# Optimization experiments

Measured on AMD Instinct MI355X. Metric: run time of the kernel, lower is better.

The kernel has to match this reference:

```python
import jax, jax.numpy as jnp
import numpy as np

B, T, D, C = 2, 2048, 1024, 10
F = D // 2 + 1  # rfft bins; permutations act on frequency bins (perm_freq=True)


def setup_inputs() -> dict:
    key = jax.random.key(0)
    ks = jax.random.split(key, 6)
    s = 1.0 / np.sqrt(D)
    x = jax.random.normal(ks[0], (B, T, D), jnp.float32)
    Wq = jax.random.normal(ks[1], (D, D), jnp.float32) * s
    Wk = jax.random.normal(ks[2], (D, D), jnp.float32) * s
    Wv = jax.random.normal(ks[3], (D, D), jnp.float32) * s
    Wo = jax.random.normal(ks[4], (D, D), jnp.float32) * s
    # buffer: torch.randn(C, F).argsort(-1) -> random permutations of freq bins
    perms = jnp.argsort(jax.random.normal(ks[5], (C, F)), axis=-1)
    return {"x": x, "Wq": Wq, "Wk": Wk, "Wv": Wv, "Wo": Wo, "perms": perms}


def reference(x, Wq, Wk, Wv, Wo, perms):
    # linear projections (nn.Linear applies x @ W.T)
    q = x @ Wq.T
    k = x @ Wk.T
    v = x @ Wv.T
    # HRR bind/unbind in rfft frequency domain
    fq = jnp.fft.rfft(q, axis=-1)  # (B,T,F) complex
    fk = jnp.fft.rfft(k, axis=-1)
    fv = jnp.fft.rfft(v, axis=-1)
    # gather permuted redundant copies of freq bins: (B,T,C,F) -> (C,B,T,F)
    fkp = jnp.moveaxis(fk[..., perms], 2, 0)
    fqp = jnp.moveaxis(fq[..., perms], 2, 0)
    # causal associative memory: cumulative sum of key*value bindings over time
    kv = jnp.cumsum(fkp * fv[None], axis=-2)  # (C,B,T,F)
    # unbind with query (circular correlation = multiply by conj), mean copies
    r = jnp.mean(kv * jnp.conj(fqp), axis=0)  # (B,T,F)
    values_hat = jnp.fft.irfft(r, n=D, axis=-1)  # (B,T,D)
    return values_hat @ Wo.T
```

## Files before the change

kernel.cpp:

```cpp
#include <hip/hip_runtime.h>
#include <math.h>

#define B_   2
#define T_   2048
#define D_   1024
#define C_   10
#define F_   513
#define NTOK (B_ * T_)
#define LF   3078
#define LFP  3136
#define KP2  1056
#define NCH  128
#define TC   (T_ / NCH)

typedef unsigned short us16;
typedef __attribute__((ext_vector_type(8))) __bf16 bf16x8;
typedef __attribute__((ext_vector_type(4))) float  f32x4;

#define O_XBF    ((size_t)0)
#define O_PREP   ((size_t)8388608)
#define O_WT     (O_PREP)
#define O_WOBF   (O_PREP + 6291456)
#define O_TCS    (O_PREP + 8388608)
#define O_RCAT   (O_PREP)
#define O_SFB    (O_PREP + 10489856)
#define O_MALLB  (O_SFB + 2162688)
#define O_MOUTB  (O_MALLB + 6303744)
#define O_FALL   (O_MOUTB + 2162688)
#define O_SSCAN  (O_FALL + 25690112)

__device__ __forceinline__ us16 f2b(float f) {
    union { float f; unsigned u; } v; v.f = f;
    unsigned r = v.u + 0x7FFFu + ((v.u >> 16) & 1u);
    return (us16)(r >> 16);
}

__device__ __forceinline__ float2 b2f2(unsigned w) {
    union { unsigned u; float f; } a, b;
    a.u = (w & 0xffffu) << 16;
    b.u = w & 0xffff0000u;
    return make_float2(a.f, b.f);
}

__device__ __forceinline__ void gl_lds16(const us16* g, us16* l) {
    __builtin_amdgcn_global_load_lds(
        (const __attribute__((address_space(1))) unsigned*)g,
        (__attribute__((address_space(3))) unsigned*)l, 16, 0, 0);
}

__global__ __launch_bounds__(256)
void hrr_prep(const float* __restrict__ x,  const float* __restrict__ Wq,
              const float* __restrict__ Wk, const float* __restrict__ Wv,
              const float* __restrict__ Wo,
              us16* __restrict__ Xbf, us16* __restrict__ WT,
              us16* __restrict__ WoBf, us16* __restrict__ Tcs,
              us16* __restrict__ Sfb) {
    __shared__ float t[32][33];
    const int bid = blockIdx.x, tid = threadIdx.x;
    if (bid < 4096) {
        int i = bid * 256 + tid;
        float4 v = ((const float4*)x)[i];
        ushort4 o;
        o.x = f2b(v.x); o.y = f2b(v.y); o.z = f2b(v.z); o.w = f2b(v.w);
        ((ushort4*)Xbf)[i] = o;
    } else if (bid < 5120) {
        int i = (bid - 4096) * 256 + tid;
        float4 v = ((const float4*)Wo)[i];
        ushort4 o;
        o.x = f2b(v.x); o.y = f2b(v.y); o.z = f2b(v.z); o.w = f2b(v.w);
        ((ushort4*)WoBf)[i] = o;
    } else if (bid < 8192) {
        const int l  = bid - 5120;
        const int bz = l >> 10, l2 = l & 1023;
        const int bx = (l2 & 31) * 32, by = (l2 >> 5) * 32;
        const float* W = (bz == 0) ? Wq : (bz == 1) ? Wk : Wv;
        us16* O = WT + (size_t)bz * D_ * D_;
        const int tx = tid & 31, ty = tid >> 5;
#pragma unroll
        for (int i = 0; i < 32; i += 8)
            t[ty + i][tx] = W[(size_t)(by + ty + i) * D_ + bx + tx];
        __syncthreads();
#pragma unroll
        for (int i = 0; i < 32; i += 8)
            O[(size_t)(bx + ty + i) * D_ + by + tx] = f2b(t[tx][ty + i]);
    } else if (bid < 12296) {
        int idx = (bid - 8192) * 256 + tid;
        int r = idx >> 10, e = idx & 1023;
        int f = r >> 1;
        float ang = (float)((f * e) & 1023) * 6.135923151542565e-3f;
        float val = (r & 1) ? -__sinf(ang) : __cosf(ang);
        float s = (f == 0 || f == 512) ? (1.0f / 1024.0f) : (2.0f / 1024.0f);
        Tcs[idx] = f2b(val);
        Sfb[idx] = f2b(s * val);
    } else {
        int idx2 = (bid - 12296) * 256 + tid;
        Sfb[1026 * 1024 + idx2] = 0;
    }
}

template <bool OUT_BF16>
__device__ __forceinline__ void gemm_core64(
    const us16* __restrict__ A, const us16* __restrict__ B, void* __restrict__ Cv,
    int M, int N, int K, int lda, int ldb, int ldc, int Ncap,
    int bm, int bn, us16* smem) {
    us16* As = smem;
    us16* Bs = smem + 8192;

    const int tid  = threadIdx.x;
    const int lane = tid & 63;
    const int wave = tid >> 6;
    const int wm = wave * 32;

    const int r0    = tid >> 2;
    const int g_lds = tid & 3;
    const int g_src = g_lds ^ ((r0 >> 1) & 3);
    const int c4    = g_src * 8;

    int rA0 = bm + r0;      if (rA0 >= M) rA0 = M - 1;
    int rA1 = bm + 64 + r0; if (rA1 >= M) rA1 = M - 1;
    int rB0 = bn + r0;      if (rB0 >= N) rB0 = N - 1;
    const us16* pA0 = A + (size_t)rA0 * lda + c4;
    const us16* pA1 = A + (size_t)rA1 * lda + c4;
    const us16* pB0 = B + (size_t)rB0 * ldb + c4;

    f32x4 acc[2][4];
#pragma unroll
    for (int i = 0; i < 2; i++)
#pragma unroll
        for (int j = 0; j < 4; j++) acc[i][j] = (f32x4){0.f, 0.f, 0.f, 0.f};

    const int fr = lane & 15;
    const int gq = ((lane >> 4) ^ ((fr >> 1) & 3)) * 8;

    const int wb = wave * 512;
#define STAGE_TILE(buf, ko)                                  \
    do {                                                     \
        us16* a_ = As + (buf) * 4096 + wb;                   \
        us16* b_ = Bs + (buf) * 2048 + wb;                   \
        gl_lds16(pA0 + (ko), a_);                            \
        gl_lds16(pA1 + (ko), a_ + 2048);                     \
        gl_lds16(pB0 + (ko), b_);                            \
    } while (0)

    STAGE_TILE(0, 0);
    __syncthreads();

    int cur = 0;
    for (int k0 = 0; k0 < K; k0 += 32) {
        const int kn = k0 + 32;
        if (kn < K) STAGE_TILE(cur ^ 1, kn);

        const us16* Ac = As + cur * 4096;
        const us16* Bc = Bs + cur * 2048;
        bf16x8 af[2], bfr[4];
#pragma unroll
        for (int i = 0; i < 2; i++)
            af[i] = *(const bf16x8*)(Ac + (wm + i * 16 + fr) * 32 + gq);
#pragma unroll
        for (int j = 0; j < 4; j++)
            bfr[j] = *(const bf16x8*)(Bc + (j * 16 + fr) * 32 + gq);
#pragma unroll
        for (int i = 0; i < 2; i++)
#pragma unroll
            for (int j = 0; j < 4; j++)
                acc[i][j] = __builtin_amdgcn_mfma_f32_16x16x32_bf16(bfr[j], af[i], acc[i][j], 0, 0, 0);

        __syncthreads();
        cur ^= 1;
    }
#undef STAGE_TILE

    const int cl  = lane & 15;
    const int rq  = (lane >> 4) * 4;
    float* lbuf = (float*)smem;
#pragma unroll
    for (int p = 0; p < 4; ++p) {
        __syncthreads();
        if (wave == p) {
#pragma unroll
            for (int i = 0; i < 2; ++i) {
                const int rl = i * 16 + cl;
#pragma unroll
                for (int j = 0; j < 4; ++j)
                    *(f32x4*)(lbuf + rl * 68 + j * 16 + rq) = acc[i][j];
            }
        }
        __syncthreads();
        const int rbase = bm + p * 32;
        if (OUT_BF16) {
            us16* C = (us16*)Cv;
            const int row = tid >> 3, col = (tid * 8) & 63;
            const int grow = rbase + row, gcol = bn + col;
            if (grow < M && gcol + 8 <= Ncap) {
                const float* s = lbuf + row * 68 + col;
                uint4 o;
                o.x = (unsigned)f2b(s[0]) | ((unsigned)f2b(s[1]) << 16);
                o.y = (unsigned)f2b(s[2]) | ((unsigned)f2b(s[3]) << 16);
                o.z = (unsigned)f2b(s[4]) | ((unsigned)f2b(s[5]) << 16);
                o.w = (unsigned)f2b(s[6]) | ((unsigned)f2b(s[7]) << 16);
                *(uint4*)(C + (size_t)grow * ldc + gcol) = o;
            }
        } else {
            float* C = (float*)Cv;
#pragma unroll
            for (int rr = 0; rr < 2; ++rr) {
                const int idx = rr * 1024 + tid * 4;
                const int row = idx >> 6, col = idx & 63;
                const int grow = rbase + row, gcol = bn + col;
                if (grow < M && gcol + 4 <= Ncap)
                    *(float4*)(C + (size_t)grow * ldc + gcol) =
                        *(const float4*)(lbuf + row * 68 + col);
            }
        }
    }
}

template <bool OUT_BF16>
__global__ __launch_bounds__(256, 4)
void hrr_gemm(const us16* __restrict__ A, const us16* __restrict__ B,
              void* __restrict__ C, int M, int N, int K,
              int lda, int ldb, int ldc, int Ncap, int swz) {
    __shared__ us16 smem[12288];
    int bx = blockIdx.x, by = blockIdx.y;
    if (swz) {
        const int gx = gridDim.x;
        const int id = bx + gx * by;
        const int q = (gx * gridDim.y) >> 3;
        const int nid = (id & 7) * q + (id >> 3);
        bx = nid % gx; by = nid / gx;
    }
    gemm_core64<OUT_BF16>(A, B, C, M, N, K, lda, ldb, ldc, Ncap,
                          by * 128, bx * 64, smem);
}

__global__ __launch_bounds__(256, 4)
void hrr_gemm_builders(const us16* __restrict__ Tcs, const us16* __restrict__ WT,
                       us16* __restrict__ MallB, const us16* __restrict__ WoBf,
                       const us16* __restrict__ Sfb, us16* __restrict__ MoutB) {
    __shared__ us16 smem[12288];
    const int z = blockIdx.z;
    if (z < 3) {
        if (blockIdx.x >= 16) return;
        gemm_core64<true>(Tcs, WT + (size_t)z * D_ * D_,
                          MallB + (size_t)z * 1026 * 1024,
                          1026, 1024, 1024, 1024, 1024, 1024, 1024,
                          blockIdx.y * 128, blockIdx.x * 64, smem);
    } else {
        if (blockIdx.y >= 8) return;
        gemm_core64<true>(WoBf, Sfb, MoutB,
                          1024, KP2, 1024, 1024, 1024, KP2, KP2,
                          blockIdx.y * 128, blockIdx.x * 64, smem);
    }
}

__global__ __launch_bounds__(512, 2)
void hrr_gemm_main(const us16* __restrict__ A, const us16* __restrict__ B,
                   us16* __restrict__ C) {
    __shared__ us16 smem[65536];
    us16* Asb = smem;
    us16* Bsb = smem + 32768;

    const int tid  = threadIdx.x;
    const int lane = tid & 63;
    const int wave = tid >> 6;

    int id = blockIdx.x + 13 * blockIdx.y;
    id = (id & 7) * 26 + (id >> 3);
    const int bx = id % 13, by = id / 13;
    const int bm = by * 256, bn = bx * 256;

    const int srow = tid >> 3;
    const int sgr  = (tid & 7) ^ (srow & 7);
    const us16* gA[4];
    const us16* gB[4];
#pragma unroll
    for (int g = 0; g < 4; ++g) {
        int ra = bm + g * 64 + srow; if (ra > NTOK - 1) ra = NTOK - 1;
        int rb = bn + g * 64 + srow; if (rb > LF - 1)   rb = LF - 1;
        gA[g] = A + (size_t)ra * 1024 + sgr * 8;
        gB[g] = B + (size_t)rb * 1024 + sgr * 8;
    }

    f32x4 acc[8][4];
#pragma unroll
    for (int i = 0; i < 8; i++)
#pragma unroll
        for (int j = 0; j < 4; j++) acc[i][j] = (f32x4){0.f, 0.f, 0.f, 0.f};

    const int wmw = (wave >> 2) * 128;
    const int wnw = (wave & 3) * 64;
    const int fr  = lane & 15;
    const int gr  = lane >> 4;
    const int l7  = lane & 7;

#define STAGE3(buf, ko)                                            \
    do {                                                           \
        us16* a_ = Asb + (buf) * 16384 + wave * 512;               \
        us16* b_ = Bsb + (buf) * 16384 + wave * 512;               \
        gl_lds16(gA[0] + (ko), a_);                                \
        gl_lds16(gA[1] + (ko), a_ + 4096);                         \
        gl_lds16(gA[2] + (ko), a_ + 8192);                         \
        gl_lds16(gA[3] + (ko), a_ + 12288);                        \
        gl_lds16(gB[0] + (ko), b_);                                \
        gl_lds16(gB[1] + (ko), b_ + 4096);                         \
        gl_lds16(gB[2] + (ko), b_ + 8192);                         \
        gl_lds16(gB[3] + (ko), b_ + 12288);                        \
    } while (0)

#define RBAR                                                       \
    do {                                                           \
        asm volatile("" ::: "memory");                             \
        __builtin_amdgcn_s_barrier();                              \
        asm volatile("" ::: "memory");                             \
    } while (0)

#define LOAD_A(ih)                                                              \
    do {                                                                        \
        _Pragma("unroll")                                                       \
        for (int i = 0; i < 4; ++i)                                             \
            _Pragma("unroll")                                                   \
            for (int ks = 0; ks < 2; ++ks)                                      \
                af[i][ks] = *(const bf16x8*)(Ac +                               \
                    (wmw + (ih) * 64 + i * 16 + fr) * 64 +                      \
                    (((ks << 2) | gr) ^ l7) * 8);                               \
    } while (0)

#define LOAD_B(jh)                                                              \
    do {                                                                        \
        _Pragma("unroll")                                                       \
        for (int j = 0; j < 2; ++j)                                             \
            _Pragma("unroll")                                                   \
            for (int ks = 0; ks < 2; ++ks)                                      \
                bfr[j][ks] = *(const bf16x8*)(Bc +                              \
                    (wnw + (jh) * 32 + j * 16 + fr) * 64 +                      \
                    (((ks << 2) | gr) ^ l7) * 8);                               \
    } while (0)

#define MFMA_Q(ih, jh)                                                          \
    do {                                                                        \
        __builtin_amdgcn_s_setprio(1);                                          \
        _Pragma("unroll")                                                       \
        for (int i = 0; i < 4; ++i)                                             \
            _Pragma("unroll")                                                   \
            for (int j = 0; j < 2; ++j)                                         \
                _Pragma("unroll")                                               \
                for (int ks = 0; ks < 2; ++ks)                                  \
                    acc[(ih) * 4 + i][(jh) * 2 + j] =                           \
                        __builtin_amdgcn_mfma_f32_16x16x32_bf16(                \
                            bfr[j][ks], af[i][ks],                              \
                            acc[(ih) * 4 + i][(jh) * 2 + j], 0, 0, 0);          \
        __builtin_amdgcn_s_setprio(0);                                          \
    } while (0)

    STAGE3(0, 0);
    asm volatile("s_waitcnt vmcnt(0)" ::: "memory");
    __builtin_amdgcn_s_barrier();
    asm volatile("" ::: "memory");

    int cur = 0;
#pragma unroll 1
    for (int t = 0; t < 16; ++t) {
        if (t < 15) STAGE3(cur ^ 1, (t + 1) * 64);

        const us16* Ac = Asb + cur * 16384;
        const us16* Bc = Bsb + cur * 16384;
        bf16x8 af[4][2], bfr[2][2];

        LOAD_A(0); LOAD_B(0); MFMA_Q(0, 0); RBAR;
        LOAD_B(1);            MFMA_Q(0, 1); RBAR;
        LOAD_A(1);            MFMA_Q(1, 1); RBAR;
        LOAD_B(0);            MFMA_Q(1, 0);
        asm volatile("s_waitcnt vmcnt(0)" ::: "memory");
        __builtin_amdgcn_s_barrier();
        asm volatile("" ::: "memory");
        cur ^= 1;
    }
#undef STAGE3
#undef LOAD_A
#undef LOAD_B
#undef MFMA_Q
#undef RBAR

    __syncthreads();
    float* lw = (float*)smem + wave * (32 * 68);
    const int cl = lane & 15;
    const int rq = (lane >> 4) * 4;
#pragma unroll
    for (int p = 0; p < 4; ++p) {
#pragma unroll
        for (int ii = 0; ii < 2; ++ii) {
            const int ifr = p * 2 + ii;
#pragma unroll
            for (int j = 0; j < 4; ++j)
                *(f32x4*)(lw + (ii * 16 + cl) * 68 + j * 16 + rq) = acc[ifr][j];
        }
        __syncthreads();
#pragma unroll
        for (int rr = 0; rr < 4; ++rr) {
            const int idx = rr * 512 + lane * 8;
            const int row = idx >> 6, col = idx & 63;
            const int grow = bm + wmw + p * 32 + row;
            const int gcol = bn + wnw + col;
            if (gcol + 8 <= LFP) {
                const float* s = lw + row * 68 + col;
                uint4 o;
                o.x = (unsigned)f2b(s[0]) | ((unsigned)f2b(s[1]) << 16);
                o.y = (unsigned)f2b(s[2]) | ((unsigned)f2b(s[3]) << 16);
                o.z = (unsigned)f2b(s[4]) | ((unsigned)f2b(s[5]) << 16);
                o.w = (unsigned)f2b(s[6]) | ((unsigned)f2b(s[7]) << 16);
                *(uint4*)(C + (size_t)grow * LFP + gcol) = o;
            }
        }
        __syncthreads();
    }
}

__global__ __launch_bounds__(256, 4)
void hrr_scan_sums(const us16* __restrict__ Fall, const int* __restrict__ perms,
                   float* __restrict__ S) {
    const int n = blockIdx.x, b = blockIdx.y, half = blockIdx.z;
    const int tid = threadIdx.x;
    const int f0 = half * 256;
    __shared__ float2 kc[F_], vc[257];

    float aR[2][C_], aI[2][C_];
    int gg[2][C_];
#pragma unroll
    for (int i = 0; i < 2; i++) {
        const int f = (i == 0) ? (f0 + tid) : 512;
        const bool act = (i == 0) || (half == 1 && tid == 0);
#pragma unroll
        for (int c = 0; c < C_; c++) {
            gg[i][c] = act ? perms[c * F_ + f] : 0;
            aR[i][c] = aI[i][c] = 0.f;
        }
    }

    const unsigned* rowb =
        (const unsigned*)(Fall + (size_t)(b * T_ + n * TC) * LFP);
    const int R32 = LFP / 2;

    unsigned rk0, rk1, rk2 = 0, rv0, rv1 = 0;
#define SFETCH(tl)                                                   \
    do {                                                             \
        const unsigned* r_ = rowb + (size_t)(tl) * R32;              \
        rk0 = r_[513 + tid];                                         \
        rk1 = r_[769 + tid];                                         \
        rv0 = r_[1026 + f0 + tid];                                   \
        if (tid == 0) { rk2 = r_[1025]; rv1 = r_[1538]; }            \
    } while (0)

    SFETCH(0);
    for (int tl = 0; tl < TC; tl++) {
        __syncthreads();
        kc[tid]       = b2f2(rk0);
        kc[256 + tid] = b2f2(rk1);
        vc[tid]       = b2f2(rv0);
        if (tid == 0) { kc[512] = b2f2(rk2); if (half) vc[256] = b2f2(rv1); }
        __syncthreads();
        if (tl + 1 < TC) SFETCH(tl + 1);
#pragma unroll
        for (int i = 0; i < 2; i++) {
            const int lv = (i == 0) ? tid : 256;
            if (i == 0 || (half == 1 && tid == 0)) {
                float2 v = vc[lv];
#pragma unroll
                for (int c = 0; c < C_; c++) {
                    float2 k = kc[gg[i][c]];
                    aR[i][c] += k.x * v.x - k.y * v.y;
                    aI[i][c] += k.x * v.y + k.y * v.x;
                }
            }
        }
    }
#undef SFETCH
#pragma unroll
    for (int i = 0; i < 2; i++) {
        const int f = (i == 0) ? (f0 + tid) : 512;
        if (i == 0 || (half == 1 && tid == 0)) {
#pragma unroll
            for (int c = 0; c < C_; c++) {
                size_t a = ((((size_t)c * B_ + b) * NCH + n) * F_ + f) * 2;
                S[a] = aR[i][c]; S[a + 1] = aI[i][c];
            }
        }
    }
}

__global__ void hrr_scan_prefix(float* __restrict__ S) {
    int tid = blockIdx.x * 256 + threadIdx.x;
    if (tid >= C_ * B_ * F_) return;
    int c = tid / (B_ * F_);
    int r = tid % (B_ * F_);
    int b = r / F_, f = r % F_;
    size_t base = (((size_t)c * B_ + b) * NCH) * F_ + f;
    float runR = 0.f, runI = 0.f;
    for (int n0 = 0; n0 < NCH; n0 += 8) {
        float tR[8], tI[8];
#pragma unroll
        for (int u = 0; u < 8; u++) {
            size_t a = (base + (size_t)(n0 + u) * F_) * 2;
            tR[u] = S[a]; tI[u] = S[a + 1];
        }
#pragma unroll
        for (int u = 0; u < 8; u++) {
            size_t a = (base + (size_t)(n0 + u) * F_) * 2;
            S[a] = runR; S[a + 1] = runI;
            runR += tR[u]; runI += tI[u];
        }
    }
}

__global__ __launch_bounds__(256, 4)
void hrr_scan_apply(const us16* __restrict__ Fall, const int* __restrict__ perms,
                    const float* __restrict__ S, us16* __restrict__ Rcat) {
    const int n = blockIdx.x, b = blockIdx.y, half = blockIdx.z;
    const int tid = threadIdx.x;
    const int f0 = half * 256;
    __shared__ float2 qc[F_], kc[F_], vc[257];

    float kvR[2][C_], kvI[2][C_];
    int gg[2][C_];
#pragma unroll
    for (int i = 0; i < 2; i++) {
        const int f = (i == 0) ? (f0 + tid) : 512;
        const bool act = (i == 0) || (half == 1 && tid == 0);
#pragma unroll
        for (int c = 0; c < C_; c++) {
            gg[i][c] = act ? perms[c * F_ + f] : 0;
            if (act) {
                size_t a = ((((size_t)c * B_ + b) * NCH + n) * F_ + f) * 2;
                kvR[i][c] = S[a]; kvI[i][c] = S[a + 1];
            } else { kvR[i][c] = 0.f; kvI[i][c] = 0.f; }
        }
    }

    const unsigned* rowb =
        (const unsigned*)(Fall + (size_t)(b * T_ + n * TC) * LFP);
    const int R32 = LFP / 2;

    unsigned rq0, rq1, rq2 = 0, rk0, rk1, rk2 = 0, rv0, rv1 = 0;
#define AFETCH(tl)                                                   \
    do {                                                             \
        const unsigned* r_ = rowb + (size_t)(tl) * R32;              \
        rq0 = r_[tid];       rq1 = r_[256 + tid];                    \
        rk0 = r_[513 + tid]; rk1 = r_[769 + tid];                    \
        rv0 = r_[1026 + f0 + tid];                                   \
        if (tid == 0) { rq2 = r_[512]; rk2 = r_[1025]; rv1 = r_[1538]; } \
    } while (0)

    AFETCH(0);
    for (int tl = 0; tl < TC; tl++) {
        const int tt = b * T_ + n * TC + tl;
        __syncthreads();
        qc[tid]       = b2f2(rq0);
        qc[256 + tid] = b2f2(rq1);
        kc[tid]       = b2f2(rk0);
        kc[256 + tid] = b2f2(rk1);
        vc[tid]       = b2f2(rv0);
        if (tid == 0) {
            qc[512] = b2f2(rq2); kc[512] = b2f2(rk2);
            if (half) vc[256] = b2f2(rv1);
        }
        __syncthreads();
        if (tl + 1 < TC) AFETCH(tl + 1);
        unsigned* out32 = (unsigned*)(Rcat + (size_t)tt * KP2);
#pragma unroll
        for (int i = 0; i < 2; i++) {
            const int f = (i == 0) ? (f0 + tid) : 512;
            const int lv = (i == 0) ? tid : 256;
            if (i == 0 || (half == 1 && tid == 0)) {
                float2 v = vc[lv];
                float accR = 0.f, accI = 0.f;
#pragma unroll
                for (int c = 0; c < C_; c++) {
                    int g = gg[i][c];
                    float2 k = kc[g];
                    float nR = kvR[i][c] + k.x * v.x - k.y * v.y;
                    float nI = kvI[i][c] + k.x * v.y + k.y * v.x;
                    kvR[i][c] = nR; kvI[i][c] = nI;
                    float2 q = qc[g];
                    accR += nR * q.x + nI * q.y;
                    accI += nI * q.x - nR * q.y;
                }
                out32[f] = (unsigned)f2b(accR * 0.1f)
                         | ((unsigned)f2b(accI * 0.1f) << 16);
            }
        }
        if (half == 0 && tid < 15)
            out32[513 + tid] = 0;
    }
#undef AFETCH
}

extern "C" void kernel_launch(void* const* d_in, const int* in_sizes, int n_in,
                              void* d_out, int out_size, void* d_ws, size_t ws_size,
                              hipStream_t stream) {
    const float* x  = (const float*)d_in[0];
    const float* Wq = (const float*)d_in[1];
    const float* Wk = (const float*)d_in[2];
    const float* Wv = (const float*)d_in[3];
    const float* Wo = (const float*)d_in[4];
    const int* perms = (const int*)d_in[5];
    float* out = (float*)d_out;

    char* ws = (char*)d_ws;
    us16* Xbf   = (us16*)(ws + O_XBF);
    us16* WT    = (us16*)(ws + O_WT);
    us16* WoBf  = (us16*)(ws + O_WOBF);
    us16* Tcs   = (us16*)(ws + O_TCS);
    us16* Sfb   = (us16*)(ws + O_SFB);
    us16* MallB = (us16*)(ws + O_MALLB);
    us16* MoutB = (us16*)(ws + O_MOUTB);
    us16* Rcat  = (us16*)(ws + O_RCAT);
    us16* Fall  = (us16*)(ws + O_FALL);
    float* Ssc  = (float*)(ws + O_SSCAN);

    hrr_prep<<<12416, 256, 0, stream>>>(x, Wq, Wk, Wv, Wo, Xbf, WT, WoBf, Tcs, Sfb);

    hrr_gemm_builders<<<dim3(17, 9, 4), 256, 0, stream>>>(Tcs, WT, MallB, WoBf, Sfb, MoutB);

    hrr_gemm_main<<<dim3(13, 16), 512, 0, stream>>>(Xbf, MallB, Fall);

    hrr_scan_sums<<<dim3(NCH, B_, 2), 256, 0, stream>>>(Fall, perms, Ssc);
    hrr_scan_prefix<<<(C_ * B_ * F_ + 255) / 256, 256, 0, stream>>>(Ssc);
    hrr_scan_apply<<<dim3(NCH, B_, 2), 256, 0, stream>>>(Fall, perms, Ssc, Rcat);

    hrr_gemm<false><<<dim3(16, 32), 256, 0, stream>>>(
        Rcat, MoutB, out, NTOK, D_, KP2, KP2, KP2, D_, D_, 1);
}
```

Measured before the change: 214.5 us.

## Switch main GEMM to 4-stage BK=32 LDS pipeline with partial vmcnt waits

Replaces the double-buffered BK=64 main loop with a four-buffer ring of BK=32 tiles, issuing global-to-LDS loads three stages ahead and waiting with partial vmcnt counts instead of draining all loads each iteration. The intra-iteration quarter barriers are removed and each wave loads all A/B fragments once per step, then runs 32 MFMAs. The LDS swizzle is changed to fit the 32-wide rows. This aims to hide global load latency better, at the cost of more loop iterations and barriers per K, and only one MFMA k-step per fragment.

```diff
diff --git a/kernel.cpp b/kernel.cpp
--- a/kernel.cpp
+++ b/kernel.cpp
@@ -269,17 +269,16 @@
     const int bx = id % 13, by = id / 13;
     const int bm = by * 256, bn = bx * 256;
 
-    const int srow = tid >> 3;
-    const int sgr  = (tid & 7) ^ (srow & 7);
-    const us16* gA[4];
-    const us16* gB[4];
-#pragma unroll
-    for (int g = 0; g < 4; ++g) {
-        int ra = bm + g * 64 + srow; if (ra > NTOK - 1) ra = NTOK - 1;
-        int rb = bn + g * 64 + srow; if (rb > LF - 1)   rb = LF - 1;
-        gA[g] = A + (size_t)ra * 1024 + sgr * 8;
-        gB[g] = B + (size_t)rb * 1024 + sgr * 8;
-    }
+    const int srow = tid >> 2;
+    const int gsrc = (tid & 3) ^ ((srow >> 1) & 3);
+    int ra0 = bm + srow;       if (ra0 > NTOK - 1) ra0 = NTOK - 1;
+    int ra1 = bm + 128 + srow; if (ra1 > NTOK - 1) ra1 = NTOK - 1;
+    int rb0 = bn + srow;       if (rb0 > LF - 1)   rb0 = LF - 1;
+    int rb1 = bn + 128 + srow; if (rb1 > LF - 1)   rb1 = LF - 1;
+    const us16* gA0 = A + (size_t)ra0 * 1024 + gsrc * 8;
+    const us16* gA1 = A + (size_t)ra1 * 1024 + gsrc * 8;
+    const us16* gB0 = B + (size_t)rb0 * 1024 + gsrc * 8;
+    const us16* gB1 = B + (size_t)rb1 * 1024 + gsrc * 8;
 
     f32x4 acc[8][4];
 #pragma unroll
@@ -290,96 +289,53 @@
     const int wmw = (wave >> 2) * 128;
     const int wnw = (wave & 3) * 64;
     const int fr  = lane & 15;
-    const int gr  = lane >> 4;
-    const int l7  = lane & 7;
-
-#define STAGE3(buf, ko)                                            \
+    const int gq8 = ((lane >> 4) ^ ((fr >> 1) & 3)) * 8;
+
+#define STAGE(buf, ko)                                             \
     do {                                                           \
-        us16* a_ = Asb + (buf) * 16384 + wave * 512;               \
-        us16* b_ = Bsb + (buf) * 16384 + wave * 512;               \
-        gl_lds16(gA[0] + (ko), a_);                                \
-        gl_lds16(gA[1] + (ko), a_ + 4096);                         \
-        gl_lds16(gA[2] + (ko), a_ + 8192);                         \
-        gl_lds16(gA[3] + (ko), a_ + 12288);                        \
-        gl_lds16(gB[0] + (ko), b_);                                \
-        gl_lds16(gB[1] + (ko), b_ + 4096);                         \
-        gl_lds16(gB[2] + (ko), b_ + 8192);                         \
-        gl_lds16(gB[3] + (ko), b_ + 12288);                        \
+        us16* a_ = Asb + (buf) * 8192 + wave * 512;                \
+        us16* b_ = Bsb + (buf) * 8192 + wave * 512;                \
+        gl_lds16(gA0 + (ko), a_);                                  \
+        gl_lds16(gA1 + (ko), a_ + 4096);                           \
+        gl_lds16(gB0 + (ko), b_);                                  \
+        gl_lds16(gB1 + (ko), b_ + 4096);                           \
     } while (0)
 
-#define RBAR                                                       \
-    do {                                                           \
-        asm volatile("" ::: "memory");                             \
-        __builtin_amdgcn_s_barrier();                              \
-        asm volatile("" ::: "memory");                             \
-    } while (0)
-
-#define LOAD_A(ih)                                                              \
-    do {                                                                        \
-        _Pragma("unroll")                                                       \
-        for (int i = 0; i < 4; ++i)                                             \
-            _Pragma("unroll")                                                   \
-            for (int ks = 0; ks < 2; ++ks)                                      \
-                af[i][ks] = *(const bf16x8*)(Ac +                               \
-                    (wmw + (ih) * 64 + i * 16 + fr) * 64 +                      \
-                    (((ks << 2) | gr) ^ l7) * 8);                               \
-    } while (0)
-
-#define LOAD_B(jh)                                                              \
-    do {                                                                        \
-        _Pragma("unroll")                                                       \
-        for (int j = 0; j < 2; ++j)                                             \
-            _Pragma("unroll")                                                   \
-            for (int ks = 0; ks < 2; ++ks)                                      \
-                bfr[j][ks] = *(const bf16x8*)(Bc +                              \
-                    (wnw + (jh) * 32 + j * 16 + fr) * 64 +                      \
-                    (((ks << 2) | gr) ^ l7) * 8);                               \
-    } while (0)
-
-#define MFMA_Q(ih, jh)                                                          \
-    do {                                                                        \
-        __builtin_amdgcn_s_setprio(1);                                          \
-        _Pragma("unroll")                                                       \
-        for (int i = 0; i < 4; ++i)                                             \
-            _Pragma("unroll")                                                   \
-            for (int j = 0; j < 2; ++j)                                         \
-                _Pragma("unroll")                                               \
-                for (int ks = 0; ks < 2; ++ks)                                  \
-                    acc[(ih) * 4 + i][(jh) * 2 + j] =                           \
-                        __builtin_amdgcn_mfma_f32_16x16x32_bf16(                \
-                            bfr[j][ks], af[i][ks],                              \
-                            acc[(ih) * 4 + i][(jh) * 2 + j], 0, 0, 0);          \
-        __builtin_amdgcn_s_setprio(0);                                          \
-    } while (0)
-
-    STAGE3(0, 0);
-    asm volatile("s_waitcnt vmcnt(0)" ::: "memory");
-    __builtin_amdgcn_s_barrier();
-    asm volatile("" ::: "memory");
-
-    int cur = 0;
+    STAGE(0, 0);
+    STAGE(1, 32);
+    STAGE(2, 64);
+
 #pragma unroll 1
-    for (int t = 0; t < 16; ++t) {
-        if (t < 15) STAGE3(cur ^ 1, (t + 1) * 64);
-
-        const us16* Ac = Asb + cur * 16384;
-        const us16* Bc = Bsb + cur * 16384;
-        bf16x8 af[4][2], bfr[2][2];
-
-        LOAD_A(0); LOAD_B(0); MFMA_Q(0, 0); RBAR;
-        LOAD_B(1);            MFMA_Q(0, 1); RBAR;
-        LOAD_A(1);            MFMA_Q(1, 1); RBAR;
-        LOAD_B(0);            MFMA_Q(1, 0);
-        asm volatile("s_waitcnt vmcnt(0)" ::: "memory");
+    for (int t = 0; t < 32; ++t) {
+        if (t < 30)       asm volatile("s_waitcnt vmcnt(8)" ::: "memory");
+        else if (t == 30) asm volatile("s_waitcnt vmcnt(4)" ::: "memory");
+        else              asm volatile("s_waitcnt vmcnt(0)" ::: "memory");
         __builtin_amdgcn_s_barrier();
         asm volatile("" ::: "memory");
-        cur ^= 1;
-    }
-#undef STAGE3
-#undef LOAD_A
-#undef LOAD_B
-#undef MFMA_Q
-#undef RBAR
+
+        if (t + 3 < 32) STAGE((t + 3) & 3, (t + 3) * 32);
+
+        const us16* Ac = Asb + (t & 3) * 8192;
+        const us16* Bc = Bsb + (t & 3) * 8192;
+        bf16x8 af[8], bfr[4];
+#pragma unroll
+        for (int i = 0; i < 8; ++i)
+            af[i] = *(const bf16x8*)(Ac + (wmw + i * 16 + fr) * 32 + gq8);
+#pragma unroll
+        for (int j = 0; j < 4; ++j)
+            bfr[j] = *(const bf16x8*)(Bc + (wnw + j * 16 + fr) * 32 + gq8);
+
+        __builtin_amdgcn_s_setprio(1);
+#pragma unroll
+        for (int i = 0; i < 8; ++i)
+#pragma unroll
+            for (int j = 0; j < 4; ++j)
+                acc[i][j] = __builtin_amdgcn_mfma_f32_16x16x32_bf16(
+                    bfr[j], af[i], acc[i][j], 0, 0, 0);
+        __builtin_amdgcn_s_setprio(0);
+        asm volatile("" ::: "memory");
+    }
+#undef STAGE
 
     __syncthreads();
     float* lw = (float*)smem + wave * (32 * 68);
```

New measurement: 213.6 us. Within noise of the previous version (-0.5%).
